# Optimization experiments

Hardware: AMD Instinct MI355X
Metric: run time of the kernel (lower is better)

The kernel has to match this reference:

```python
import jax, jax.numpy as jnp
import numpy as np

N, E, D, H = 100000, 20000, 64, 4
NNZ = 500000
NEG_SLOPE_ATT = 0.2   # PyG HypergraphConv attention leaky_relu slope
NEG_SLOPE_FFN = 0.01  # nn.LeakyReLU default
LN_EPS = 1e-5


def setup_inputs() -> dict:
    key = jax.random.key(0)
    ks = jax.random.split(key, 10)
    s = 0.05
    return {
        "x": jax.random.normal(ks[0], (N, D), jnp.float32),
        "adj_row": jax.random.randint(ks[1], (NNZ,), 0, N),
        "adj_col": jax.random.randint(ks[2], (NNZ,), 0, E),
        "adj_val": jax.random.uniform(ks[3], (NNZ,), jnp.float32) + 0.1,
        "num_edges": E,
        "lin_w": jax.random.normal(ks[4], (H * D, D), jnp.float32) * s,
        "att": jax.random.normal(ks[5], (1, H, 2 * D), jnp.float32) * s,
        "bias": jnp.zeros((D,), jnp.float32),
        "ln1_g": jnp.ones((D,), jnp.float32),
        "ln1_b": jnp.zeros((D,), jnp.float32),
        "ln2_g": jnp.ones((D,), jnp.float32),
        "ln2_b": jnp.zeros((D,), jnp.float32),
        "w1": jax.random.normal(ks[6], (D, D), jnp.float32) * s,
        "b1": jnp.zeros((D,), jnp.float32),
        "w2": jax.random.normal(ks[7], (D, D), jnp.float32) * s,
        "b2": jnp.zeros((D,), jnp.float32),
    }


def _layer_norm(x, g, b):
    mu = jnp.mean(x, axis=-1, keepdims=True)
    var = jnp.mean((x - mu) ** 2, axis=-1, keepdims=True)
    return (x - mu) * jax.lax.rsqrt(var + LN_EPS) * g + b


def _hypergraph_layer(x, adj_row, adj_col, adj_val, num_edges,
                      lin_w, att, bias, ln1_g, ln1_b, ln2_g, ln2_b,
                      w1, b1, w2, b2):
    n = x.shape[0]
    # --- get_hyperedge_representation: omega = diag(1/colsum) @ H^T @ x ---
    colsum = jax.ops.segment_sum(adj_val, adj_col, num_segments=num_edges)  # [E]
    omega = jax.ops.segment_sum(adj_val[:, None] * x[adj_row], adj_col,
                                num_segments=num_edges) / colsum[:, None]  # [E, D]
    # --- HypergraphConv (use_attention=True, concat=False) ---
    xh = (x @ lin_w.T).reshape(n, H, D)              # [N, H, D]
    eh = (omega @ lin_w.T).reshape(num_edges, H, D)  # [E, H, D]
    att_x, att_e = att[0, :, :D], att[0, :, D:]      # [H, D] each
    s_n = jnp.einsum('nhd,hd->nh', xh, att_x)        # [N, H]
    s_e = jnp.einsum('ehd,hd->eh', eh, att_e)        # [E, H]
    alpha = jax.nn.leaky_relu(s_n[adj_row] + s_e[adj_col], NEG_SLOPE_ATT)  # [NNZ, H]
    # softmax over incidences grouped by hyperedge (attention_mode='node')
    amax = jax.ops.segment_max(alpha, adj_col, num_segments=num_edges)
    ea = jnp.exp(alpha - amax[adj_col])
    alpha = ea / jax.ops.segment_sum(ea, adj_col, num_segments=num_edges)[adj_col]
    # degree normalizations D (node) and B (hyperedge)
    d_deg = jax.ops.segment_sum(adj_val[adj_col], adj_row, num_segments=n)
    d_inv = jnp.where(d_deg > 0, 1.0 / d_deg, 0.0)
    b_deg = jax.ops.segment_sum(jnp.ones_like(adj_val), adj_col, num_segments=num_edges)
    b_inv = jnp.where(b_deg > 0, 1.0 / b_deg, 0.0)
    # pass 1: nodes -> hyperedges  (norm_i = B at target edge)
    msg1 = b_inv[adj_col][:, None, None] * xh[adj_row] * alpha[:, :, None]
    edge_out = jax.ops.segment_sum(msg1, adj_col, num_segments=num_edges)  # [E,H,D]
    # pass 2: hyperedges -> nodes  (norm_i = D at target node)
    msg2 = d_inv[adj_row][:, None, None] * edge_out[adj_col] * alpha[:, :, None]
    node_out = jax.ops.segment_sum(msg2, adj_row, num_segments=n)  # [N,H,D]
    conv = jnp.mean(node_out, axis=1) + bias  # concat=False -> head mean
    # --- residual + norm + FFN (Linear, Linear, LeakyReLU) ---
    h = _layer_norm(x + conv, ln1_g, ln1_b)
    ffn = jax.nn.leaky_relu((h @ w1.T + b1) @ w2.T + b2, NEG_SLOPE_FFN)
    return _layer_norm(h + ffn, ln2_g, ln2_b)


def reference(x, adj_row, adj_col, adj_val, num_edges, lin_w, att, bias,
              ln1_g, ln1_b, ln2_g, ln2_b, w1, b1, w2, b2):
    return _hypergraph_layer(x, adj_row, adj_col, adj_val, num_edges,
                             lin_w, att, bias, ln1_g, ln1_b, ln2_g, ln2_b,
                             w1, b1, w2, b2)
```

## Files before the change

### kernel.cpp

```cpp
#include <hip/hip_runtime.h>

#define N_NODES 100000
#define N_EDGES 20000
#define DIM 64
#define HEADS 4
#define NNZ_ 500000
#define LNEPS 1e-5f

__device__ __forceinline__ float wsum64(float v){
#pragma unroll
  for (int off = 32; off; off >>= 1) v += __shfl_xor(v, off);
  return v;
}
__device__ __forceinline__ float wmax64(float v){
#pragma unroll
  for (int off = 32; off; off >>= 1) v = fmaxf(v, __shfl_xor(v, off));
  return v;
}
__device__ __forceinline__ float lrelu2(float a){ return a > 0.f ? a : 0.2f*a; }

__device__ __forceinline__ unsigned bfpack(float a, float b){
  unsigned ua = __float_as_uint(a), ub = __float_as_uint(b);
  ua += 0x7fffu + ((ua >> 16) & 1u);
  ub += 0x7fffu + ((ub >> 16) & 1u);
  return (ua >> 16) | (ub & 0xffff0000u);
}

__global__ __launch_bounds__(256) void k_hist(const int* __restrict__ row,
                                              const int* __restrict__ col,
                                              const float* __restrict__ val,
                                              int* __restrict__ ecnt, int* __restrict__ ncnt,
                                              float* __restrict__ colsum, float* __restrict__ ddeg){
  int i = blockIdx.x*256 + threadIdx.x;
  if (i >= NNZ_) return;
  int c = col[i], r = row[i];
  atomicAdd(&ecnt[c], 1);
  atomicAdd(&ncnt[r], 1);
  atomicAdd(&colsum[c], val[i]);
  atomicAdd(&ddeg[r], val[c]);
}

__global__ __launch_bounds__(1024) void k_scanA(const int* __restrict__ cnt,
                                                int* __restrict__ ptr,
                                                int* __restrict__ bsum, int n){
  __shared__ int wsums[16];
  int idx = blockIdx.x*1024 + threadIdx.x;
  int lane = threadIdx.x & 63, wid = threadIdx.x >> 6;
  int v = (idx < n) ? cnt[idx] : 0;
  int s = v;
#pragma unroll
  for (int off = 1; off < 64; off <<= 1){
    int t = __shfl_up(s, off);
    if (lane >= off) s += t;
  }
  if (lane == 63) wsums[wid] = s;
  __syncthreads();
  if (wid == 0 && lane < 16){
    int ws = wsums[lane];
    int t = ws;
#pragma unroll
    for (int off = 1; off < 16; off <<= 1){
      int u = __shfl_up(t, off);
      if (lane >= off) t += u;
    }
    wsums[lane] = t - ws;
  }
  __syncthreads();
  if (idx < n) ptr[idx] = wsums[wid] + s - v;
  if (threadIdx.x == 1023) bsum[blockIdx.x] = wsums[15] + s;
}

__global__ __launch_bounds__(256) void k_scanB(int* __restrict__ bsum, int nb,
                                               int* __restrict__ ptr, int n){
  __shared__ int sh[256];
  int t = threadIdx.x;
  int v = (t < nb) ? bsum[t] : 0;
  sh[t] = v;
  __syncthreads();
  for (int off = 1; off < 256; off <<= 1){
    int u = (t >= off) ? sh[t-off] : 0;
    __syncthreads();
    sh[t] += u;
    __syncthreads();
  }
  if (t < nb) bsum[t] = sh[t] - v;
  if (t == nb-1) ptr[n] = sh[t];
}

__global__ __launch_bounds__(1024) void k_scanC(int* __restrict__ ptr,
                                                const int* __restrict__ bsum, int n){
  int idx = blockIdx.x*1024 + threadIdx.x;
  if (idx < n) ptr[idx] += bsum[blockIdx.x];
}

__global__ __launch_bounds__(256) void k_scatter(const int* __restrict__ row,
                                                 const int* __restrict__ col,
                                                 const float* __restrict__ val,
                                                 const int* __restrict__ colptr,
                                                 const int* __restrict__ rowptr,
                                                 int* __restrict__ ecur, int* __restrict__ ncur,
                                                 int* __restrict__ rowC, float* __restrict__ valC,
                                                 int* __restrict__ rposC, int* __restrict__ colR){
  int i = blockIdx.x*256 + threadIdx.x;
  if (i >= NNZ_) return;
  int c = col[i], r = row[i];
  int p = atomicAdd(&ecur[c], 1);
  int q = atomicAdd(&ncur[r], 1);
  int cpos = colptr[c] + p;
  int rpos = rowptr[r] + q;
  rowC[cpos] = r;
  valC[cpos] = val[i];
  rposC[cpos] = rpos;
  colR[rpos] = c;
}

__global__ __launch_bounds__(256) void k_watt(const float* __restrict__ lin_w,
                                              const float* __restrict__ att,
                                              float* __restrict__ wattx,
                                              float* __restrict__ watte){
  int j = threadIdx.x;
  int h = j >> 6;
  float sx = 0.f, se = 0.f;
#pragma unroll
  for (int d = 0; d < DIM; ++d){
    float w = lin_w[(h*DIM + d)*DIM + (j & 63)];
    sx = fmaf(att[h*2*DIM + d],       w, sx);
    se = fmaf(att[h*2*DIM + DIM + d], w, se);
  }
  wattx[j] = sx;
  watte[j] = se;
}

__global__ __launch_bounds__(256) void k_wfold(const float* __restrict__ w1,
                                               const float* __restrict__ w2,
                                               const float* __restrict__ b1,
                                               const float* __restrict__ b2,
                                               float* __restrict__ Wf,
                                               float* __restrict__ bp){
  int tid = threadIdx.x;
#pragma unroll
  for (int m = 0; m < 16; ++m){
    int idx = m*256 + tid;
    int o = idx >> 6, k = idx & 63;
    float s = 0.f;
#pragma unroll
    for (int i = 0; i < 64; ++i)
      s = fmaf(w2[o*64 + i], w1[i*64 + k], s);
    Wf[idx] = s;
  }
  if (tid < 64){
    float s = b2[tid];
#pragma unroll
    for (int i = 0; i < 64; ++i)
      s = fmaf(w2[tid*64 + i], b1[i], s);
    bp[tid] = s;
  }
}

__global__ __launch_bounds__(256) void k_pre(const float* __restrict__ x,
                                             const float* __restrict__ wattx,
                                             const float* __restrict__ watte,
                                             float4* __restrict__ snpe){
  int lane = threadIdx.x & 63, wid = threadIdx.x >> 6;
  int n = blockIdx.x*4 + wid;
  if (n >= N_NODES) return;
  float xv = x[(size_t)n*DIM + lane];
  float s0 = wsum64(xv*wattx[lane]);
  float s1 = wsum64(xv*wattx[64+lane]);
  float s2 = wsum64(xv*wattx[128+lane]);
  float s3 = wsum64(xv*wattx[192+lane]);
  float p0 = wsum64(xv*watte[lane]);
  float p1 = wsum64(xv*watte[64+lane]);
  float p2 = wsum64(xv*watte[128+lane]);
  float p3 = wsum64(xv*watte[192+lane]);
  if (lane == 0){
    snpe[2*(size_t)n    ] = make_float4(s0,s1,s2,s3);
    snpe[2*(size_t)n + 1] = make_float4(p0,p1,p2,p3);
  }
}

__global__ __launch_bounds__(256) void k_soft(const int* __restrict__ colptr,
                                              const int* __restrict__ rowC,
                                              const float* __restrict__ valC,
                                              const int* __restrict__ rposC,
                                              const float4* __restrict__ snpe,
                                              const float* __restrict__ colsum,
                                              float4* __restrict__ alphaC,
                                              float4* __restrict__ alphaR){
  int lane = threadIdx.x & 63, wid = threadIdx.x >> 6;
  int e = blockIdx.x*4 + wid;
  if (e >= N_EDGES) return;
  int s = colptr[e], cnt = colptr[e+1] - s;
  if (cnt == 0) return;
  float rcs = 1.0f / colsum[e];

  if (cnt <= 64){
    bool act = lane < cnt;
    int rp = 0; float v = 0.f;
    float4 snv = make_float4(0,0,0,0), p = make_float4(0,0,0,0);
    if (act){
      int r = rowC[s+lane];
      v = valC[s+lane];
      rp = rposC[s+lane];
      snv = snpe[2*(size_t)r];
      p   = snpe[2*(size_t)r + 1];
    }
    float se0 = wsum64(v*p.x)*rcs, se1 = wsum64(v*p.y)*rcs,
          se2 = wsum64(v*p.z)*rcs, se3 = wsum64(v*p.w)*rcs;
    float t0 = act ? lrelu2(snv.x+se0) : -1e30f;
    float t1 = act ? lrelu2(snv.y+se1) : -1e30f;
    float t2 = act ? lrelu2(snv.z+se2) : -1e30f;
    float t3 = act ? lrelu2(snv.w+se3) : -1e30f;
    float m0 = wmax64(t0), m1 = wmax64(t1), m2 = wmax64(t2), m3 = wmax64(t3);
    float e0 = act ? __expf(t0-m0) : 0.f;
    float e1 = act ? __expf(t1-m1) : 0.f;
    float e2 = act ? __expf(t2-m2) : 0.f;
    float e3 = act ? __expf(t3-m3) : 0.f;
    float q0 = wsum64(e0), q1 = wsum64(e1), q2 = wsum64(e2), q3 = wsum64(e3);
    if (act){
      float4 a = make_float4(e0/q0, e1/q1, e2/q2, e3/q3);
      alphaC[s+lane] = a;
      alphaR[rp] = a;
    }
    return;
  }
  float a0=0,a1=0,a2=0,a3=0;
  for (int base = 0; base < cnt; base += 64){
    int j = s + base + lane;
    if (base + lane < cnt){
      int r = rowC[j]; float v = valC[j];
      float4 p = snpe[2*(size_t)r + 1];
      a0 = fmaf(v,p.x,a0); a1 = fmaf(v,p.y,a1); a2 = fmaf(v,p.z,a2); a3 = fmaf(v,p.w,a3);
    }
  }
  float se0 = wsum64(a0)*rcs, se1 = wsum64(a1)*rcs, se2 = wsum64(a2)*rcs, se3 = wsum64(a3)*rcs;
  float m0=-1e30f,m1=-1e30f,m2=-1e30f,m3=-1e30f;
  for (int base = 0; base < cnt; base += 64){
    int j = s + base + lane;
    if (base + lane < cnt){
      float4 snv = snpe[2*(size_t)rowC[j]];
      m0 = fmaxf(m0, lrelu2(snv.x+se0)); m1 = fmaxf(m1, lrelu2(snv.y+se1));
      m2 = fmaxf(m2, lrelu2(snv.z+se2)); m3 = fmaxf(m3, lrelu2(snv.w+se3));
    }
  }
  m0 = wmax64(m0); m1 = wmax64(m1); m2 = wmax64(m2); m3 = wmax64(m3);
  float q0=0,q1=0,q2=0,q3=0;
  for (int base = 0; base < cnt; base += 64){
    int j = s + base + lane;
    if (base + lane < cnt){
      float4 snv = snpe[2*(size_t)rowC[j]];
      float e0 = __expf(lrelu2(snv.x+se0)-m0), e1 = __expf(lrelu2(snv.y+se1)-m1);
      float e2 = __expf(lrelu2(snv.z+se2)-m2), e3 = __expf(lrelu2(snv.w+se3)-m3);
      q0+=e0; q1+=e1; q2+=e2; q3+=e3;
      alphaC[j] = make_float4(e0,e1,e2,e3);
    }
  }
  q0 = wsum64(q0); q1 = wsum64(q1); q2 = wsum64(q2); q3 = wsum64(q3);
  float r0 = 1.f/q0, r1 = 1.f/q1, r2 = 1.f/q2, r3 = 1.f/q3;
  for (int base = 0; base < cnt; base += 64){
    int j = s + base + lane;
    if (base + lane < cnt){
      float4 a = alphaC[j];
      a = make_float4(a.x*r0, a.y*r1, a.z*r2, a.w*r3);
      alphaC[j] = a;
      alphaR[rposC[j]] = a;
    }
  }
}

__global__ __launch_bounds__(256) void k_agg(const int* __restrict__ colptr,
                                             const int* __restrict__ rowC,
                                             const float4* __restrict__ alphaC,
                                             const float* __restrict__ x,
                                             float* __restrict__ agg){
  int lane = threadIdx.x & 63, wid = threadIdx.x >> 6;
  int e = blockIdx.x*4 + wid;
  if (e >= N_EDGES) return;
  int s = colptr[e], cnt = colptr[e+1] - s;
  float acc0=0,acc1=0,acc2=0,acc3=0;
  for (int base = 0; base < cnt; base += 64){
    int m = cnt - base; if (m > 64) m = 64;
    int r = 0; float4 al = make_float4(0,0,0,0);
    if (lane < m){ r = rowC[s+base+lane]; al = alphaC[s+base+lane]; }
#pragma unroll 8
    for (int j = 0; j < m; ++j){
      int rj = __shfl(r, j);
      float b0 = __shfl(al.x, j), b1 = __shfl(al.y, j),
            b2 = __shfl(al.z, j), b3 = __shfl(al.w, j);
      float xv = x[(size_t)rj*DIM + lane];
      acc0 = fmaf(b0, xv, acc0); acc1 = fmaf(b1, xv, acc1);
      acc2 = fmaf(b2, xv, acc2); acc3 = fmaf(b3, xv, acc3);
    }
  }
  float binv = cnt > 0 ? 1.0f/(float)cnt : 0.f;
  size_t b = (size_t)e*256;
  agg[b       + lane] = acc0*binv;
  agg[b +  64 + lane] = acc1*binv;
  agg[b + 128 + lane] = acc2*binv;
  agg[b + 192 + lane] = acc3*binv;
}

__global__ __launch_bounds__(256) void k_eoT(const float* __restrict__ agg,
                                             const float* __restrict__ lin_w,
                                             unsigned short* __restrict__ eoTb){
  __shared__ float L[16*260];
  int lane = threadIdx.x & 63, h = threadIdx.x >> 6;
  float w[64];
  const float4* wr = (const float4*)(lin_w + ((size_t)h*64 + lane)*64);
#pragma unroll
  for (int k = 0; k < 16; ++k){
    float4 t = wr[k];
    w[4*k] = t.x; w[4*k+1] = t.y; w[4*k+2] = t.z; w[4*k+3] = t.w;
  }
  int e0 = blockIdx.x*16;
  for (int el = 0; el < 16; ++el){
    float av = agg[(size_t)(e0+el)*256 + h*64 + lane];
    float o = 0.f;
#pragma unroll
    for (int k = 0; k < 64; ++k) o = fmaf(__shfl(av, k), w[k], o);
    L[el*260 + lane*4 + h] = o;
  }
  __syncthreads();
  int tid = threadIdx.x;
#pragma unroll
  for (int p = 0; p < 4; ++p){
    int el = p*4 + (tid >> 6);
    int l = tid & 63;
    const float* Lr = &L[el*260 + l*4];
    uint2 v;
    v.x = bfpack(Lr[0], Lr[1]);
    v.y = bfpack(Lr[2], Lr[3]);
    *(uint2*)(eoTb + (size_t)(e0+el)*256 + l*4) = v;
  }
}

__global__ __launch_bounds__(256) void k_final2(const float* __restrict__ x,
                                                const int* __restrict__ rowptr,
                                                const int* __restrict__ colR,
                                                const float4* __restrict__ alphaR,
                                                const unsigned short* __restrict__ eoTb,
                                                const float* __restrict__ ddeg,
                                                const float* __restrict__ bias,
                                                const float* __restrict__ g1,
                                                const float* __restrict__ b1g,
                                                const float* __restrict__ g2,
                                                const float* __restrict__ b2g,
                                                const float* __restrict__ Wf,
                                                const float* __restrict__ bp,
                                                float* __restrict__ out){
  int lane = threadIdx.x & 63, wid = threadIdx.x >> 6;
  float w[64];
  const float4* wr = (const float4*)(Wf + (size_t)lane*64);
#pragma unroll
  for (int k = 0; k < 16; ++k){
    float4 t = wr[k];
    w[4*k] = t.x; w[4*k+1] = t.y; w[4*k+2] = t.z; w[4*k+3] = t.w;
  }
  float biasv = bias[lane], bpv = bp[lane];
  float g1v = g1[lane], b1gv = b1g[lane], g2v = g2[lane], b2gv = b2g[lane];

  int nbase = blockIdx.x*16 + wid*4;
  int p0 = rowptr[nbase], p1 = rowptr[nbase+1], p2 = rowptr[nbase+2],
      p3 = rowptr[nbase+3], p4 = rowptr[nbase+4];
  int total = p4 - p0;
  int cj0 = p1-p0, cj1 = p2-p1, cj2 = p3-p2, cj3 = p4-p3;
  int oj0 = 0, oj1 = p1-p0, oj2 = p2-p0, oj3 = p3-p0;

  float acc[4][4];
#pragma unroll
  for (int j = 0; j < 4; ++j)
#pragma unroll
    for (int h = 0; h < 4; ++h) acc[j][h] = 0.f;

  if (total <= 64){
    int ce = 0; float4 alv = make_float4(0,0,0,0);
    if (lane < total){ ce = colR[p0+lane]; alv = alphaR[p0+lane]; }
    int maxc = max(max(cj0,cj1), max(cj2,cj3));
    int cj[4] = {cj0,cj1,cj2,cj3};
    int oj[4] = {oj0,oj1,oj2,oj3};
    for (int k = 0; k < maxc; ++k){
#pragma unroll
      for (int j = 0; j < 4; ++j){
        if (k < cj[j]){
          int idx = oj[j] + k;
          int ci = __shfl(ce, idx);
          float q0 = __shfl(alv.x, idx), q1 = __shfl(alv.y, idx),
                q2 = __shfl(alv.z, idx), q3 = __shfl(alv.w, idx);
          uint2 v = *(const uint2*)(eoTb + (size_t)ci*256 + lane*4);
          float v0 = __uint_as_float(v.x << 16);
          float v1 = __uint_as_float(v.x & 0xffff0000u);
          float v2 = __uint_as_float(v.y << 16);
          float v3 = __uint_as_float(v.y & 0xffff0000u);
          acc[j][0] = fmaf(v0, q0, acc[j][0]);
          acc[j][1] = fmaf(v1, q1, acc[j][1]);
          acc[j][2] = fmaf(v2, q2, acc[j][2]);
          acc[j][3] = fmaf(v3, q3, acc[j][3]);
        }
      }
    }
  } else {
    int sj[4] = {p0, p1, p2, p3};
    int cj[4] = {cj0,cj1,cj2,cj3};
#pragma unroll
    for (int j = 0; j < 4; ++j){
      int s = sj[j], cnt = cj[j];
      for (int base = 0; base < cnt; base += 64){
        int m = cnt - base; if (m > 64) m = 64;
        int c = 0; float4 al = make_float4(0,0,0,0);
        if (lane < m){ c = colR[s+base+lane]; al = alphaR[s+base+lane]; }
        for (int i = 0; i < m; ++i){
          int ci = __shfl(c, i);
          float q0 = __shfl(al.x, i), q1 = __shfl(al.y, i),
                q2 = __shfl(al.z, i), q3 = __shfl(al.w, i);
          uint2 v = *(const uint2*)(eoTb + (size_t)ci*256 + lane*4);
          float v0 = __uint_as_float(v.x << 16);
          float v1 = __uint_as_float(v.x & 0xffff0000u);
          float v2 = __uint_as_float(v.y << 16);
          float v3 = __uint_as_float(v.y & 0xffff0000u);
          acc[j][0] = fmaf(v0, q0, acc[j][0]);
          acc[j][1] = fmaf(v1, q1, acc[j][1]);
          acc[j][2] = fmaf(v2, q2, acc[j][2]);
          acc[j][3] = fmaf(v3, q3, acc[j][3]);
        }
      }
    }
  }

  float hs[4];
#pragma unroll
  for (int j = 0; j < 4; ++j){
    int n = nbase + j;
    float dd = ddeg[n];
    float dinv = dd > 0.f ? 0.25f/dd : 0.f;
    float conv = (acc[j][0]+acc[j][1]+acc[j][2]+acc[j][3])*dinv;
    float t = x[(size_t)n*DIM + lane] + conv + biasv;
    float mu = wsum64(t) * (1.f/64.f);
    float dv = t - mu;
    float var = wsum64(dv*dv) * (1.f/64.f);
    hs[j] = dv * rsqrtf(var + LNEPS) * g1v + b1gv;
  }

  float a0 = bpv, a1 = bpv, a2 = bpv, a3 = bpv;
#pragma unroll
  for (int k = 0; k < 64; ++k){
    a0 = fmaf(__shfl(hs[0], k), w[k], a0);
    a1 = fmaf(__shfl(hs[1], k), w[k], a1);
    a2 = fmaf(__shfl(hs[2], k), w[k], a2);
    a3 = fmaf(__shfl(hs[3], k), w[k], a3);
  }

  float fa[4] = {a0, a1, a2, a3};
#pragma unroll
  for (int j = 0; j < 4; ++j){
    int n = nbase + j;
    float ffn = fa[j] > 0.f ? fa[j] : 0.01f*fa[j];
    float t2 = hs[j] + ffn;
    float mu2 = wsum64(t2) * (1.f/64.f);
    float dv2 = t2 - mu2;
    float var2 = wsum64(dv2*dv2) * (1.f/64.f);
    out[(size_t)n*DIM + lane] = dv2 * rsqrtf(var2 + LNEPS) * g2v + b2gv;
  }
}

extern "C" void kernel_launch(void* const* d_in, const int* in_sizes, int n_in,
                              void* d_out, int out_size, void* d_ws, size_t ws_size,
                              hipStream_t stream){
  const float* x     = (const float*)d_in[0];
  const int*   row   = (const int*)d_in[1];
  const int*   col   = (const int*)d_in[2];
  const float* val   = (const float*)d_in[3];
  const float* lin_w = (const float*)d_in[5];
  const float* att   = (const float*)d_in[6];
  const float* bias  = (const float*)d_in[7];
  const float* g1    = (const float*)d_in[8];
  const float* b1g   = (const float*)d_in[9];
  const float* g2    = (const float*)d_in[10];
  const float* b2g   = (const float*)d_in[11];
  const float* w1    = (const float*)d_in[12];
  const float* b1    = (const float*)d_in[13];
  const float* w2    = (const float*)d_in[14];
  const float* b2    = (const float*)d_in[15];
  float* out = (float*)d_out;
  float* ws  = (float*)d_ws;

  constexpr size_t E = N_EDGES, Nn = N_NODES;
  constexpr size_t o_ecnt   = 0;
  constexpr size_t o_ncnt   = o_ecnt + E;
  constexpr size_t o_ecur   = o_ncnt + Nn;
  constexpr size_t o_ncur   = o_ecur + E;
  constexpr size_t o_colsum = o_ncur + Nn;
  constexpr size_t o_ddeg   = o_colsum + E;
  constexpr size_t ZEND     = o_ddeg + Nn;
  constexpr size_t o_colptr = ZEND;
  constexpr size_t o_rowptr = o_colptr + E + 4;
  constexpr size_t o_bsumE  = o_rowptr + Nn + 4;
  constexpr size_t o_bsumN  = o_bsumE + 256;
  constexpr size_t o_rowC   = o_bsumN + 256;
  constexpr size_t o_valC   = o_rowC + NNZ_;
  constexpr size_t o_rposC  = o_valC + NNZ_;
  constexpr size_t o_colR   = o_rposC + NNZ_;
  constexpr size_t o_wattx  = o_colR + NNZ_;
  constexpr size_t o_watte  = o_wattx + 256;
  constexpr size_t o_Wf     = o_watte + 256;
  constexpr size_t o_bp     = o_Wf + 4096;
  constexpr size_t o_snpe   = o_bp + 64;
  constexpr size_t o_alphaC = o_snpe + 8*Nn;
  constexpr size_t o_alphaR = o_alphaC + 4*(size_t)NNZ_;
  constexpr size_t o_agg    = o_alphaR + 4*(size_t)NNZ_;
  constexpr size_t o_eo     = o_agg + 256*E;

  int*    ecnt   = (int*)(ws + o_ecnt);
  int*    ncnt   = (int*)(ws + o_ncnt);
  int*    ecur   = (int*)(ws + o_ecur);
  int*    ncur   = (int*)(ws + o_ncur);
  float*  colsum = ws + o_colsum;
  float*  ddeg   = ws + o_ddeg;
  int*    colptr = (int*)(ws + o_colptr);
  int*    rowptr = (int*)(ws + o_rowptr);
  int*    bsumE  = (int*)(ws + o_bsumE);
  int*    bsumN  = (int*)(ws + o_bsumN);
  int*    rowC   = (int*)(ws + o_rowC);
  float*  valC   = ws + o_valC;
  int*    rposC  = (int*)(ws + o_rposC);
  int*    colR   = (int*)(ws + o_colR);
  float*  wattx  = ws + o_wattx;
  float*  watte  = ws + o_watte;
  float*  Wf     = ws + o_Wf;
  float*  bp     = ws + o_bp;
  float4* snpe   = (float4*)(ws + o_snpe);
  float4* alphaC = (float4*)(ws + o_alphaC);
  float4* alphaR = (float4*)(ws + o_alphaR);
  float*  agg    = ws + o_agg;
  unsigned short* eoTb = (unsigned short*)(ws + o_eo);

  hipMemsetAsync(ws, 0, ZEND*sizeof(float), stream);

  k_hist<<<(NNZ_+255)/256, 256, 0, stream>>>(row, col, val, ecnt, ncnt, colsum, ddeg);

  int nbE = (int)((E + 1023)/1024);
  int nbN = (int)((Nn + 1023)/1024);
  k_scanA<<<nbE, 1024, 0, stream>>>(ecnt, colptr, bsumE, (int)E);
  k_scanB<<<1, 256, 0, stream>>>(bsumE, nbE, colptr, (int)E);
  k_scanC<<<nbE, 1024, 0, stream>>>(colptr, bsumE, (int)E);
  k_scanA<<<nbN, 1024, 0, stream>>>(ncnt, rowptr, bsumN, (int)Nn);
  k_scanB<<<1, 256, 0, stream>>>(bsumN, nbN, rowptr, (int)Nn);
  k_scanC<<<nbN, 1024, 0, stream>>>(rowptr, bsumN, (int)Nn);

  k_scatter<<<(NNZ_+255)/256, 256, 0, stream>>>(row, col, val, colptr, rowptr,
                                                ecur, ncur, rowC, valC, rposC, colR);

  k_watt<<<1, 256, 0, stream>>>(lin_w, att, wattx, watte);
  k_wfold<<<1, 256, 0, stream>>>(w1, w2, b1, b2, Wf, bp);
  k_pre<<<(int)((Nn+3)/4), 256, 0, stream>>>(x, wattx, watte, snpe);
  k_soft<<<(int)((E+3)/4), 256, 0, stream>>>(colptr, rowC, valC, rposC, snpe, colsum, alphaC, alphaR);
  k_agg<<<(int)((E+3)/4), 256, 0, stream>>>(colptr, rowC, alphaC, x, agg);
  k_eoT<<<(int)(E/16), 256, 0, stream>>>(agg, lin_w, eoTb);
  k_final2<<<(int)(Nn/16), 256, 0, stream>>>(x, rowptr, colR, alphaR, eoTb, ddeg,
                                             bias, g1, b1g, g2, b2g, Wf, bp, out);
}
```

Before: 526.3 us.

## Fuse softmax and edge aggregation kernels; unroll gathers in final node kernel

Merges the per-hyperedge attention softmax and the weighted node-feature aggregation into one kernel. For edges with at most 64 members, the alphas stay in registers and are broadcast by shuffle, so the alphaC write and re-read and a separate kernel launch go away. The final node kernel now processes each node's incidences in groups of four independent bf16 gathers, and issues the x, ddeg and index loads before the weight load, to expose more memory-level parallelism. Empty edges no longer write zeros into agg, which is only safe because no node references them.

```diff
diff --git a/kernel.cpp b/kernel.cpp
--- a/kernel.cpp
+++ b/kernel.cpp
@@ -179,27 +179,30 @@
   }
 }
 
-__global__ __launch_bounds__(256) void k_soft(const int* __restrict__ colptr,
-                                              const int* __restrict__ rowC,
-                                              const float* __restrict__ valC,
-                                              const int* __restrict__ rposC,
-                                              const float4* __restrict__ snpe,
-                                              const float* __restrict__ colsum,
-                                              float4* __restrict__ alphaC,
-                                              float4* __restrict__ alphaR){
+__global__ __launch_bounds__(256) void k_softagg(const int* __restrict__ colptr,
+                                                 const int* __restrict__ rowC,
+                                                 const float* __restrict__ valC,
+                                                 const int* __restrict__ rposC,
+                                                 const float4* __restrict__ snpe,
+                                                 const float* __restrict__ colsum,
+                                                 const float* __restrict__ x,
+                                                 float4* __restrict__ alphaC,
+                                                 float4* __restrict__ alphaR,
+                                                 float* __restrict__ agg){
   int lane = threadIdx.x & 63, wid = threadIdx.x >> 6;
   int e = blockIdx.x*4 + wid;
   if (e >= N_EDGES) return;
   int s = colptr[e], cnt = colptr[e+1] - s;
   if (cnt == 0) return;
   float rcs = 1.0f / colsum[e];
+  float acc0=0,acc1=0,acc2=0,acc3=0;
 
   if (cnt <= 64){
     bool act = lane < cnt;
-    int rp = 0; float v = 0.f;
+    int r = 0, rp = 0; float v = 0.f;
     float4 snv = make_float4(0,0,0,0), p = make_float4(0,0,0,0);
     if (act){
-      int r = rowC[s+lane];
+      r = rowC[s+lane];
       v = valC[s+lane];
       rp = rposC[s+lane];
       snv = snpe[2*(size_t)r];
@@ -217,82 +220,85 @@
     float e2 = act ? __expf(t2-m2) : 0.f;
     float e3 = act ? __expf(t3-m3) : 0.f;
     float q0 = wsum64(e0), q1 = wsum64(e1), q2 = wsum64(e2), q3 = wsum64(e3);
-    if (act){
-      float4 a = make_float4(e0/q0, e1/q1, e2/q2, e3/q3);
-      alphaC[s+lane] = a;
-      alphaR[rp] = a;
-    }
-    return;
-  }
-  float a0=0,a1=0,a2=0,a3=0;
-  for (int base = 0; base < cnt; base += 64){
-    int j = s + base + lane;
-    if (base + lane < cnt){
-      int r = rowC[j]; float v = valC[j];
-      float4 p = snpe[2*(size_t)r + 1];
-      a0 = fmaf(v,p.x,a0); a1 = fmaf(v,p.y,a1); a2 = fmaf(v,p.z,a2); a3 = fmaf(v,p.w,a3);
-    }
-  }
-  float se0 = wsum64(a0)*rcs, se1 = wsum64(a1)*rcs, se2 = wsum64(a2)*rcs, se3 = wsum64(a3)*rcs;
-  float m0=-1e30f,m1=-1e30f,m2=-1e30f,m3=-1e30f;
-  for (int base = 0; base < cnt; base += 64){
-    int j = s + base + lane;
-    if (base + lane < cnt){
-      float4 snv = snpe[2*(size_t)rowC[j]];
-      m0 = fmaxf(m0, lrelu2(snv.x+se0)); m1 = fmaxf(m1, lrelu2(snv.y+se1));
-      m2 = fmaxf(m2, lrelu2(snv.z+se2)); m3 = fmaxf(m3, lrelu2(snv.w+se3));
-    }
-  }
-  m0 = wmax64(m0); m1 = wmax64(m1); m2 = wmax64(m2); m3 = wmax64(m3);
-  float q0=0,q1=0,q2=0,q3=0;
-  for (int base = 0; base < cnt; base += 64){
-    int j = s + base + lane;
-    if (base + lane < cnt){
-      float4 snv = snpe[2*(size_t)rowC[j]];
-      float e0 = __expf(lrelu2(snv.x+se0)-m0), e1 = __expf(lrelu2(snv.y+se1)-m1);
-      float e2 = __expf(lrelu2(snv.z+se2)-m2), e3 = __expf(lrelu2(snv.w+se3)-m3);
-      q0+=e0; q1+=e1; q2+=e2; q3+=e3;
-      alphaC[j] = make_float4(e0,e1,e2,e3);
-    }
-  }
-  q0 = wsum64(q0); q1 = wsum64(q1); q2 = wsum64(q2); q3 = wsum64(q3);
-  float r0 = 1.f/q0, r1 = 1.f/q1, r2 = 1.f/q2, r3 = 1.f/q3;
-  for (int base = 0; base < cnt; base += 64){
-    int j = s + base + lane;
-    if (base + lane < cnt){
-      float4 a = alphaC[j];
-      a = make_float4(a.x*r0, a.y*r1, a.z*r2, a.w*r3);
-      alphaC[j] = a;
-      alphaR[rposC[j]] = a;
-    }
-  }
-}
-
-__global__ __launch_bounds__(256) void k_agg(const int* __restrict__ colptr,
-                                             const int* __restrict__ rowC,
-                                             const float4* __restrict__ alphaC,
-                                             const float* __restrict__ x,
-                                             float* __restrict__ agg){
-  int lane = threadIdx.x & 63, wid = threadIdx.x >> 6;
-  int e = blockIdx.x*4 + wid;
-  if (e >= N_EDGES) return;
-  int s = colptr[e], cnt = colptr[e+1] - s;
-  float acc0=0,acc1=0,acc2=0,acc3=0;
-  for (int base = 0; base < cnt; base += 64){
-    int m = cnt - base; if (m > 64) m = 64;
-    int r = 0; float4 al = make_float4(0,0,0,0);
-    if (lane < m){ r = rowC[s+base+lane]; al = alphaC[s+base+lane]; }
-#pragma unroll 8
-    for (int j = 0; j < m; ++j){
-      int rj = __shfl(r, j);
-      float b0 = __shfl(al.x, j), b1 = __shfl(al.y, j),
-            b2 = __shfl(al.z, j), b3 = __shfl(al.w, j);
-      float xv = x[(size_t)rj*DIM + lane];
-      acc0 = fmaf(b0, xv, acc0); acc1 = fmaf(b1, xv, acc1);
-      acc2 = fmaf(b2, xv, acc2); acc3 = fmaf(b3, xv, acc3);
-    }
-  }
-  float binv = cnt > 0 ? 1.0f/(float)cnt : 0.f;
+    float4 a = make_float4(e0/q0, e1/q1, e2/q2, e3/q3);
+    if (act) alphaR[rp] = a;
+
+    for (int k0 = 0; k0 < cnt; k0 += 4){
+      float xu[4], b0[4], b1[4], b2[4], b3[4];
+#pragma unroll
+      for (int u = 0; u < 4; ++u){
+        int idx = k0 + u;
+        bool a2 = idx < cnt;
+        int rj = __shfl(r, idx);
+        xu[u] = a2 ? x[(size_t)rj*DIM + lane] : 0.f;
+        b0[u] = __shfl(a.x, idx); b1[u] = __shfl(a.y, idx);
+        b2[u] = __shfl(a.z, idx); b3[u] = __shfl(a.w, idx);
+      }
+#pragma unroll
+      for (int u = 0; u < 4; ++u){
+        acc0 = fmaf(b0[u], xu[u], acc0); acc1 = fmaf(b1[u], xu[u], acc1);
+        acc2 = fmaf(b2[u], xu[u], acc2); acc3 = fmaf(b3[u], xu[u], acc3);
+      }
+    }
+  } else {
+    float a0=0,a1=0,a2=0,a3=0;
+    for (int base = 0; base < cnt; base += 64){
+      int j = s + base + lane;
+      if (base + lane < cnt){
+        int r = rowC[j]; float v = valC[j];
+        float4 p = snpe[2*(size_t)r + 1];
+        a0 = fmaf(v,p.x,a0); a1 = fmaf(v,p.y,a1); a2 = fmaf(v,p.z,a2); a3 = fmaf(v,p.w,a3);
+      }
+    }
+    float se0 = wsum64(a0)*rcs, se1 = wsum64(a1)*rcs, se2 = wsum64(a2)*rcs, se3 = wsum64(a3)*rcs;
+    float m0=-1e30f,m1=-1e30f,m2=-1e30f,m3=-1e30f;
+    for (int base = 0; base < cnt; base += 64){
+      int j = s + base + lane;
+      if (base + lane < cnt){
+        float4 snv = snpe[2*(size_t)rowC[j]];
+        m0 = fmaxf(m0, lrelu2(snv.x+se0)); m1 = fmaxf(m1, lrelu2(snv.y+se1));
+        m2 = fmaxf(m2, lrelu2(snv.z+se2)); m3 = fmaxf(m3, lrelu2(snv.w+se3));
+      }
+    }
+    m0 = wmax64(m0); m1 = wmax64(m1); m2 = wmax64(m2); m3 = wmax64(m3);
+    float q0=0,q1=0,q2=0,q3=0;
+    for (int base = 0; base < cnt; base += 64){
+      int j = s + base + lane;
+      if (base + lane < cnt){
+        float4 snv = snpe[2*(size_t)rowC[j]];
+        float e0 = __expf(lrelu2(snv.x+se0)-m0), e1 = __expf(lrelu2(snv.y+se1)-m1);
+        float e2 = __expf(lrelu2(snv.z+se2)-m2), e3 = __expf(lrelu2(snv.w+se3)-m3);
+        q0+=e0; q1+=e1; q2+=e2; q3+=e3;
+        alphaC[j] = make_float4(e0,e1,e2,e3);
+      }
+    }
+    q0 = wsum64(q0); q1 = wsum64(q1); q2 = wsum64(q2); q3 = wsum64(q3);
+    float r0 = 1.f/q0, r1 = 1.f/q1, r2 = 1.f/q2, r3 = 1.f/q3;
+    for (int base = 0; base < cnt; base += 64){
+      int j = s + base + lane;
+      if (base + lane < cnt){
+        float4 av = alphaC[j];
+        av = make_float4(av.x*r0, av.y*r1, av.z*r2, av.w*r3);
+        alphaC[j] = av;
+        alphaR[rposC[j]] = av;
+      }
+    }
+    for (int base = 0; base < cnt; base += 64){
+      int m = cnt - base; if (m > 64) m = 64;
+      int r = 0; float4 al = make_float4(0,0,0,0);
+      if (lane < m){ r = rowC[s+base+lane]; al = alphaC[s+base+lane]; }
+      for (int j = 0; j < m; ++j){
+        int rj = __shfl(r, j);
+        float c0 = __shfl(al.x, j), c1 = __shfl(al.y, j),
+              c2 = __shfl(al.z, j), c3 = __shfl(al.w, j);
+        float xv = x[(size_t)rj*DIM + lane];
+        acc0 = fmaf(c0, xv, acc0); acc1 = fmaf(c1, xv, acc1);
+        acc2 = fmaf(c2, xv, acc2); acc3 = fmaf(c3, xv, acc3);
+      }
+    }
+  }
+
+  float binv = 1.0f/(float)cnt;
   size_t b = (size_t)e*256;
   agg[b       + lane] = acc0*binv;
   agg[b +  64 + lane] = acc1*binv;
@@ -349,22 +355,27 @@
                                                 const float* __restrict__ bp,
                                                 float* __restrict__ out){
   int lane = threadIdx.x & 63, wid = threadIdx.x >> 6;
-  float w[64];
-  const float4* wr = (const float4*)(Wf + (size_t)lane*64);
-#pragma unroll
-  for (int k = 0; k < 16; ++k){
-    float4 t = wr[k];
-    w[4*k] = t.x; w[4*k+1] = t.y; w[4*k+2] = t.z; w[4*k+3] = t.w;
-  }
-  float biasv = bias[lane], bpv = bp[lane];
-  float g1v = g1[lane], b1gv = b1g[lane], g2v = g2[lane], b2gv = b2g[lane];
-
   int nbase = blockIdx.x*16 + wid*4;
   int p0 = rowptr[nbase], p1 = rowptr[nbase+1], p2 = rowptr[nbase+2],
       p3 = rowptr[nbase+3], p4 = rowptr[nbase+4];
   int total = p4 - p0;
-  int cj0 = p1-p0, cj1 = p2-p1, cj2 = p3-p2, cj3 = p4-p3;
-  int oj0 = 0, oj1 = p1-p0, oj2 = p2-p0, oj3 = p3-p0;
+
+  int ce = 0; float4 alv = make_float4(0,0,0,0);
+  if (lane < total && total <= 64){ ce = colR[p0+lane]; alv = alphaR[p0+lane]; }
+
+  float xv[4];
+#pragma unroll
+  for (int j = 0; j < 4; ++j) xv[j] = x[(size_t)(nbase+j)*DIM + lane];
+  float dd0 = ddeg[nbase], dd1 = ddeg[nbase+1], dd2 = ddeg[nbase+2], dd3 = ddeg[nbase+3];
+  float w[64];
+  const float4* wr = (const float4*)(Wf + (size_t)lane*64);
+#pragma unroll
+  for (int k = 0; k < 16; ++k){
+    float4 t = wr[k];
+    w[4*k] = t.x; w[4*k+1] = t.y; w[4*k+2] = t.z; w[4*k+3] = t.w;
+  }
+  float biasv = bias[lane], bpv = bp[lane];
+  float g1v = g1[lane], b1gv = b1g[lane], g2v = g2[lane], b2gv = b2g[lane];
 
   float acc[4][4];
 #pragma unroll
@@ -373,34 +384,39 @@
     for (int h = 0; h < 4; ++h) acc[j][h] = 0.f;
 
   if (total <= 64){
-    int ce = 0; float4 alv = make_float4(0,0,0,0);
-    if (lane < total){ ce = colR[p0+lane]; alv = alphaR[p0+lane]; }
-    int maxc = max(max(cj0,cj1), max(cj2,cj3));
-    int cj[4] = {cj0,cj1,cj2,cj3};
-    int oj[4] = {oj0,oj1,oj2,oj3};
-    for (int k = 0; k < maxc; ++k){
-#pragma unroll
-      for (int j = 0; j < 4; ++j){
-        if (k < cj[j]){
-          int idx = oj[j] + k;
+    int cj[4] = {p1-p0, p2-p1, p3-p2, p4-p3};
+    int oj[4] = {0, p1-p0, p2-p0, p3-p0};
+#pragma unroll
+    for (int j = 0; j < 4; ++j){
+      int cnt = cj[j], off = oj[j];
+      for (int k0 = 0; k0 < cnt; k0 += 4){
+        uint2 v[4]; float b0[4], b1[4], b2[4], b3[4];
+#pragma unroll
+        for (int u = 0; u < 4; ++u){
+          int idx = off + k0 + u;
+          bool act = (k0 + u) < cnt;
           int ci = __shfl(ce, idx);
-          float q0 = __shfl(alv.x, idx), q1 = __shfl(alv.y, idx),
-                q2 = __shfl(alv.z, idx), q3 = __shfl(alv.w, idx);
-          uint2 v = *(const uint2*)(eoTb + (size_t)ci*256 + lane*4);
-          float v0 = __uint_as_float(v.x << 16);
-          float v1 = __uint_as_float(v.x & 0xffff0000u);
-          float v2 = __uint_as_float(v.y << 16);
-          float v3 = __uint_as_float(v.y & 0xffff0000u);
-          acc[j][0] = fmaf(v0, q0, acc[j][0]);
-          acc[j][1] = fmaf(v1, q1, acc[j][1]);
-          acc[j][2] = fmaf(v2, q2, acc[j][2]);
-          acc[j][3] = fmaf(v3, q3, acc[j][3]);
+          uint2 z; z.x = 0u; z.y = 0u;
+          v[u] = act ? *(const uint2*)(eoTb + (size_t)ci*256 + lane*4) : z;
+          b0[u] = __shfl(alv.x, idx); b1[u] = __shfl(alv.y, idx);
+          b2[u] = __shfl(alv.z, idx); b3[u] = __shfl(alv.w, idx);
+        }
+#pragma unroll
+        for (int u = 0; u < 4; ++u){
+          float v0 = __uint_as_float(v[u].x << 16);
+          float v1 = __uint_as_float(v[u].x & 0xffff0000u);
+          float v2 = __uint_as_float(v[u].y << 16);
+          float v3 = __uint_as_float(v[u].y & 0xffff0000u);
+          acc[j][0] = fmaf(v0, b0[u], acc[j][0]);
+          acc[j][1] = fmaf(v1, b1[u], acc[j][1]);
+          acc[j][2] = fmaf(v2, b2[u], acc[j][2]);
+          acc[j][3] = fmaf(v3, b3[u], acc[j][3]);
         }
       }
     }
   } else {
     int sj[4] = {p0, p1, p2, p3};
-    int cj[4] = {cj0,cj1,cj2,cj3};
+    int cj[4] = {p1-p0, p2-p1, p3-p2, p4-p3};
 #pragma unroll
     for (int j = 0; j < 4; ++j){
       int s = sj[j], cnt = cj[j];
@@ -426,14 +442,14 @@
     }
   }
 
+  float ddv[4] = {dd0, dd1, dd2, dd3};
   float hs[4];
 #pragma unroll
   for (int j = 0; j < 4; ++j){
-    int n = nbase + j;
-    float dd = ddeg[n];
+    float dd = ddv[j];
     float dinv = dd > 0.f ? 0.25f/dd : 0.f;
     float conv = (acc[j][0]+acc[j][1]+acc[j][2]+acc[j][3])*dinv;
-    float t = x[(size_t)n*DIM + lane] + conv + biasv;
+    float t = xv[j] + conv + biasv;
     float mu = wsum64(t) * (1.f/64.f);
     float dv = t - mu;
     float var = wsum64(dv*dv) * (1.f/64.f);
@@ -552,8 +568,8 @@
   k_watt<<<1, 256, 0, stream>>>(lin_w, att, wattx, watte);
   k_wfold<<<1, 256, 0, stream>>>(w1, w2, b1, b2, Wf, bp);
   k_pre<<<(int)((Nn+3)/4), 256, 0, stream>>>(x, wattx, watte, snpe);
-  k_soft<<<(int)((E+3)/4), 256, 0, stream>>>(colptr, rowC, valC, rposC, snpe, colsum, alphaC, alphaR);
-  k_agg<<<(int)((E+3)/4), 256, 0, stream>>>(colptr, rowC, alphaC, x, agg);
+  k_softagg<<<(int)((E+3)/4), 256, 0, stream>>>(colptr, rowC, valC, rposC, snpe, colsum,
+                                                x, alphaC, alphaR, agg);
   k_eoT<<<(int)(E/16), 256, 0, stream>>>(agg, lin_w, eoTb);
   k_final2<<<(int)(Nn/16), 256, 0, stream>>>(x, rowptr, colR, alphaR, eoTb, ddeg,
                                              bias, g1, b1g, g2, b2g, Wf, bp, out);
```

Result: faster. 498.6 us (-5.3%).
